# Kernel optimization log

Hardware: AMD Instinct MI355X
Metric: run time of the kernel (lower is better)

Reference implementation:

```python
import jax, jax.numpy as jnp
import numpy as np

B, T, S_ENC, D = 2, 1024, 1024, 2048
NQ, NKV, H = 16, 8, 256
EPS = 1e-6
CAP = 50.0
SCALE = 0.0625  # query_pre_attn_scalar = head_dim**-0.5
BASE = 10000
K_MASK = -2.3819763e+38


def rms_norm(x, scale, eps=EPS):
    var = jnp.mean(jnp.square(x), axis=-1, keepdims=True)
    return x * jax.lax.rsqrt(var + eps) * (1.0 + scale)


def apply_rope(x, positions, base=BASE):
    # x: [B, L, N, H], positions: [B, L] float. rope_proportion=1.0 -> full head.
    head_dim = x.shape[-1]
    timescale = base ** (2.0 / head_dim * jnp.arange(head_dim // 2, dtype=jnp.float32))
    sinusoid = positions[..., None] / timescale  # [B, L, H/2]
    sinusoid = sinusoid[..., None, :]            # [B, L, 1, H/2]
    sin, cos = jnp.sin(sinusoid), jnp.cos(sinusoid)
    x1, x2 = jnp.split(x, 2, axis=-1)
    return jnp.concatenate([x1 * cos - x2 * sin, x2 * cos + x1 * sin], axis=-1).astype(x.dtype)


def setup_inputs() -> dict:
    key = jax.random.key(0)
    ks = jax.random.split(key, 6)
    hidden_states = jax.random.normal(ks[0], (B, T, D), jnp.float32)
    encoder_hidden_states = jax.random.normal(ks[1], (B, S_ENC, D), jnp.float32)
    position_ids = jnp.broadcast_to(jnp.arange(T, dtype=jnp.int32), (B, T))
    causal = jnp.tril(jnp.ones((T, T), bool))
    merged = jnp.concatenate([causal, jnp.ones((T, S_ENC), bool)], axis=-1)
    merged_attention_mask = jnp.broadcast_to(merged[None, None], (B, 1, T, T + S_ENC))
    q_w = jax.random.normal(ks[2], (NQ, D, H), jnp.float32) * 0.02
    k_w = jax.random.normal(ks[3], (NKV, D, H), jnp.float32) * 0.02
    v_w = jax.random.normal(ks[4], (NKV, D, H), jnp.float32) * 0.02
    o_w = jax.random.normal(ks[5], (NQ, H, D), jnp.float32) * 0.02
    q_scale = jnp.zeros((H,), jnp.float32)
    k_scale = jnp.zeros((H,), jnp.float32)
    return {
        'hidden_states': hidden_states,
        'encoder_hidden_states': encoder_hidden_states,
        'position_ids': position_ids,
        'merged_attention_mask': merged_attention_mask,
        'q_w': q_w, 'k_w': k_w, 'v_w': v_w, 'o_w': o_w,
        'q_scale': q_scale, 'k_scale': k_scale,
    }


def reference(hidden_states, encoder_hidden_states, position_ids, merged_attention_mask,
              q_w, k_w, v_w, o_w, q_scale, k_scale):
    # Fused QKV projections
    q = jnp.einsum('BTD,NDH->BTNH', hidden_states, q_w)
    self_k = jnp.einsum('BTD,NDH->BTNH', hidden_states, k_w)
    self_v = jnp.einsum('BTD,NDH->BTNH', hidden_states, v_w)
    # QK RMSNorm
    q = rms_norm(q, q_scale)
    self_k = rms_norm(self_k, k_scale)
    # RoPE on decoder-side q/k only
    pos = position_ids.astype(jnp.float32)
    q = apply_rope(q, pos)
    self_k = apply_rope(self_k, pos)
    # Cross KV (no RoPE, k-norm applied)
    cross_k = rms_norm(jnp.einsum('BTD,NDH->BTNH', encoder_hidden_states, k_w), k_scale)
    cross_v = jnp.einsum('BTD,NDH->BTNH', encoder_hidden_states, v_w)
    # Merge KV: [B, T+S_enc, NKV, H]
    k = jnp.concatenate([self_k, cross_k], axis=1)
    v = jnp.concatenate([self_v, cross_v], axis=1)
    q = q * SCALE
    # GQA: group query heads over kv heads
    G = NQ // NKV
    qg = q.reshape(B, T, NKV, G, H)
    logits = jnp.einsum('BTKGH,BSKH->BKGTS', qg, k)
    # Logit soft-cap
    logits = CAP * jnp.tanh(logits / CAP)
    mask = merged_attention_mask[:, 0][:, None, None]  # [B,1,1,T,S_comb]
    logits = jnp.where(mask, logits, K_MASK)
    probs = jax.nn.softmax(logits, axis=-1)
    out = jnp.einsum('BKGTS,BSKH->BTKGH', probs, v).reshape(B, T, NQ, H)
    return jnp.einsum('BTNH,NHD->BTD', out, o_w)
```

## Files before the change

kernel.cpp:

```cpp
#include <hip/hip_runtime.h>
#include <hip/hip_bf16.h>
#include <stdint.h>

typedef __hip_bfloat16 bf16;
typedef __attribute__((ext_vector_type(8))) short bv8;
typedef __attribute__((ext_vector_type(4))) float f32x4;


__device__ __forceinline__ f32x4 mfma16(bv8 a, bv8 b, f32x4 c) {
  return __builtin_amdgcn_mfma_f32_16x16x32_bf16(a, b, c, 0, 0, 0);
}

__device__ __forceinline__ void gload16(const void* g, void* lds) {
  __builtin_amdgcn_global_load_lds((const __attribute__((address_space(1))) void*)g,
                                   (__attribute__((address_space(3))) void*)lds, 16, 0, 0);
}

__device__ __forceinline__ void storeC(float* p, float v) { *p = v; }
__device__ __forceinline__ void storeC(bf16* p, float v) { *p = __float2bfloat16(v); }

__global__ void cast2_f32_bf16(const float* __restrict__ a, const float* __restrict__ b,
                               bf16* __restrict__ da, bf16* __restrict__ db, int n4each) {
  int i = blockIdx.x * blockDim.x + threadIdx.x;
  const float* s;
  bf16* d;
  if (i < n4each) { s = a; d = da; }
  else            { s = b; d = db; i -= n4each; }
  float4 v = reinterpret_cast<const float4*>(s)[i];
  bf16 t[4] = {__float2bfloat16(v.x), __float2bfloat16(v.y),
               __float2bfloat16(v.z), __float2bfloat16(v.w)};
  reinterpret_cast<uint64_t*>(d)[i] = *reinterpret_cast<uint64_t*>(t);
}

__global__ void transpose_cast_qkv(const float* __restrict__ q_w, const float* __restrict__ k_w,
                                   const float* __restrict__ v_w, bf16* __restrict__ dst) {
  __shared__ float tile[32][33];
  const int z = blockIdx.z;
  const float* s = (z < 16) ? q_w + (size_t)z * 524288
                 : (z < 24) ? k_w + (size_t)(z - 16) * 524288
                            : v_w + (size_t)(z - 24) * 524288;
  bf16* d = dst + (size_t)z * 524288;
  const int R = 2048, C = 256;
  const int c0 = blockIdx.x * 32, r0 = blockIdx.y * 32;
  const int x = threadIdx.x, y = threadIdx.y;
#pragma unroll
  for (int i = 0; i < 32; i += 8)
    tile[y + i][x] = s[(size_t)(r0 + y + i) * C + c0 + x];
  __syncthreads();
#pragma unroll
  for (int i = 0; i < 32; i += 8)
    d[(size_t)(c0 + y + i) * R + r0 + x] = __float2bfloat16(tile[x][y + i]);
}

__global__ void transpose_cast(const float* __restrict__ src, bf16* __restrict__ dst,
                               int R, int C) {
  __shared__ float tile[32][33];
  const float* s = src;
  bf16* d = dst;
  const int c0 = blockIdx.x * 32, r0 = blockIdx.y * 32;
  const int x = threadIdx.x, y = threadIdx.y;
#pragma unroll
  for (int i = 0; i < 32; i += 8)
    tile[y + i][x] = s[(size_t)(r0 + y + i) * C + c0 + x];
  __syncthreads();
#pragma unroll
  for (int i = 0; i < 32; i += 8)
    d[(size_t)(c0 + y + i) * R + r0 + x] = __float2bfloat16(tile[x][y + i]);
}

__global__ void transpose_v2(const bf16* __restrict__ vself, const bf16* __restrict__ vcross,
                             bf16* __restrict__ dst) {
  __shared__ bf16 tile[32][33];
  const int z = blockIdx.z;
  const int zz = z & 15, b = zz >> 3, kvh = zz & 7;
  const bool cross = z >= 16;
  const bf16* srcb = cross ? vcross : vself;
  const int src_ld = cross ? 4096 : 8192;
  const int t0 = cross ? 1024 : 0;
  const bf16* s = srcb + (size_t)(b * 1024) * src_ld + kvh * 256;
  bf16* d = dst + (size_t)(zz * 256) * 2048 + t0;
  const int h0 = blockIdx.x * 32, tt0 = blockIdx.y * 32;
  const int x = threadIdx.x, y = threadIdx.y;
#pragma unroll
  for (int i = 0; i < 32; i += 8)
    tile[y + i][x] = s[(size_t)(tt0 + y + i) * src_ld + h0 + x];
  __syncthreads();
#pragma unroll
  for (int i = 0; i < 32; i += 8)
    d[(size_t)(h0 + y + i) * 2048 + tt0 + x] = tile[x][y + i];
}

template <typename CT>
__device__ __forceinline__ void gemm_body(const bf16* __restrict__ A, const bf16* __restrict__ Bt,
                                          CT* __restrict__ C, int N, int K,
                                          int m0, int n0, int kbase, int ksteps) {
  __shared__ __align__(16) bf16 As[128 * 32];
  __shared__ __align__(16) bf16 Bs[128 * 32];
  const int tid = threadIdx.x;
  const int w = tid >> 6, l = tid & 63;
  const int wr = w >> 1, wc = w & 1;
  const int l15 = l & 15, lhi = l >> 4;
  const bf16* ag = A + (size_t)(m0 + (tid >> 2)) * K + kbase + (tid & 3) * 8;
  const bf16* bg = Bt + (size_t)(n0 + (tid >> 2)) * K + kbase + (tid & 3) * 8;
  bf16* asw = As + w * 512;
  bf16* bsw = Bs + w * 512;
  f32x4 acc[4][4] = {};
  for (int k0 = 0; k0 < ksteps; k0 += 32) {
    gload16(ag + k0, asw);
    gload16(ag + (size_t)64 * K + k0, asw + 2048);
    gload16(bg + k0, bsw);
    gload16(bg + (size_t)64 * K + k0, bsw + 2048);
    asm volatile("s_waitcnt vmcnt(0)" ::: "memory");
    __syncthreads();
    bv8 af[4], bfv[4];
#pragma unroll
    for (int m = 0; m < 4; ++m)
      af[m] = *reinterpret_cast<const bv8*>(As + (wr * 64 + m * 16 + l15) * 32 + lhi * 8);
#pragma unroll
    for (int n = 0; n < 4; ++n)
      bfv[n] = *reinterpret_cast<const bv8*>(Bs + (wc * 64 + n * 16 + l15) * 32 + lhi * 8);
#pragma unroll
    for (int m = 0; m < 4; ++m)
#pragma unroll
      for (int n = 0; n < 4; ++n)
        acc[m][n] = mfma16(af[m], bfv[n], acc[m][n]);
    __syncthreads();
  }
  const int r0 = m0 + wr * 64 + lhi * 4;
  const int c0 = n0 + wc * 64 + l15;
#pragma unroll
  for (int m = 0; m < 4; ++m)
#pragma unroll
    for (int n = 0; n < 4; ++n) {
      f32x4 v = acc[m][n];
#pragma unroll
      for (int j = 0; j < 4; ++j)
        storeC(&C[(size_t)(r0 + m * 16 + j) * N + c0 + n * 16], v[j]);
    }
}

__launch_bounds__(256)
__global__ void gemm_proj(const bf16* __restrict__ hid, const bf16* __restrict__ enc,
                          const bf16* __restrict__ wqkvt, bf16* __restrict__ cself,
                          bf16* __restrict__ ccross) {
  const int bx = blockIdx.x;
  const bool cross = bx >= 64;
  const bf16* A = cross ? enc : hid;
  const bf16* Bt = cross ? wqkvt + 8388608 : wqkvt;
  bf16* C = cross ? ccross : cself;
  const int N = cross ? 4096 : 8192;
  const int n0 = (cross ? bx - 64 : bx) * 128;
  gemm_body<bf16>(A, Bt, C, N, 2048, blockIdx.y * 128, n0, 0, 2048);
}

__launch_bounds__(256)
__global__ void gemm_osplit(const bf16* __restrict__ A, const bf16* __restrict__ Bt,
                            float* __restrict__ out, float* __restrict__ p1) {
  float* C = blockIdx.z ? p1 : out;
  gemm_body<float>(A, Bt, C, 2048, 4096, blockIdx.y * 128, blockIdx.x * 128,
                   blockIdx.z * 2048, 2048);
}

__global__ void add_inplace(float* __restrict__ out, const float* __restrict__ p1, int n4) {
  int i = blockIdx.x * blockDim.x + threadIdx.x;
  if (i >= n4) return;
  float4 a = reinterpret_cast<float4*>(out)[i];
  float4 b = reinterpret_cast<const float4*>(p1)[i];
  a.x += b.x; a.y += b.y; a.z += b.z; a.w += b.w;
  reinterpret_cast<float4*>(out)[i] = a;
}

template <bool ROPE>
__launch_bounds__(256)
__global__ void norm_finalize(const bf16* __restrict__ src, int src_ld, int src_col0,
                              const float* __restrict__ scale,
                              const int* __restrict__ pos_ids,
                              bf16* __restrict__ dst, int nheads, int dst_S, int dst_t0,
                              float mul) {
  const int gid = blockIdx.x * 4 + (threadIdx.x >> 6);
  const int l = threadIdx.x & 63;
  const int token = gid / nheads;
  const int n = gid - token * nheads;
  const int b = token >> 10;
  const int t = token & 1023;
  const size_t soff = (size_t)token * src_ld + src_col0 + n * 256 + l * 4;
  bf16 xb[4];
  *reinterpret_cast<uint64_t*>(xb) = *reinterpret_cast<const uint64_t*>(src + soff);
  float x[4];
#pragma unroll
  for (int c = 0; c < 4; ++c) x[c] = __bfloat162float(xb[c]);
  float ss = x[0] * x[0] + x[1] * x[1] + x[2] * x[2] + x[3] * x[3];
#pragma unroll
  for (int d = 1; d < 64; d <<= 1) ss += __shfl_xor(ss, d);
  const float r = rsqrtf(ss * (1.0f / 256.0f) + 1e-6f);
  float v[4];
#pragma unroll
  for (int c = 0; c < 4; ++c) v[c] = x[c] * r * (1.0f + scale[l * 4 + c]);
  if (ROPE) {
    const float pos = (float)pos_ids[token];
    float o[4];
#pragma unroll
    for (int c = 0; c < 4; ++c) {
      const int j = (l & 31) * 4 + c;
      const float inv_ts = exp2f(-(float)j * 0.10381025296523007f);
      const float arg = pos * inv_ts;
      const float sj = sinf(arg), cj = cosf(arg);
      const float partner = __shfl_xor(v[c], 32);
      o[c] = (l < 32) ? (v[c] * cj - partner * sj) : (v[c] * cj + partner * sj);
    }
#pragma unroll
    for (int c = 0; c < 4; ++c) v[c] = o[c];
  }
  bf16 ob[4];
#pragma unroll
  for (int c = 0; c < 4; ++c) ob[c] = __float2bfloat16(v[c] * mul);
  const size_t doff = ((size_t)((b * nheads + n) * dst_S + dst_t0 + t)) * 256 + l * 4;
  *reinterpret_cast<uint64_t*>(dst + doff) = *reinterpret_cast<uint64_t*>(ob);
}

__launch_bounds__(512, 2)
__global__ void attn_kernel(const bf16* __restrict__ qb, const bf16* __restrict__ kb,
                            const bf16* __restrict__ vt, bf16* __restrict__ attn_out) {
  __shared__ __align__(16) bf16 Ks[2][64 * 256];
  __shared__ __align__(16) bf16 Vs[2][256 * 64];
  __shared__ __align__(16) bf16 pbuf[2][64 * 72];
  __shared__ float rsb[2][2][2][2][4][4];
  const int lin = blockIdx.x + 16 * blockIdx.y;
  const int kvc = (lin & 7) | (((lin >> 7) & 1) << 3);
  const int qt  = (lin >> 3) & 15;
  const int b = kvc >> 3, kvh = kvc & 7;
  const int tid = threadIdx.x, w = tid >> 6, l = tid & 63;
  const int g = w >> 2, qsp = (w >> 1) & 1, sh = w & 1, hq = w & 3;
  const int n = kvh * 2 + g;
  const int l15 = l & 15, lhi = l >> 4;
  const int xr = (l15 & 7) << 4;

  const bf16* kbase = kb + (size_t)(b * 8 + kvh) * 2048 * 256;
  const bf16* vbase = vt + (size_t)(b * 8 + kvh) * 256 * 2048;

  const bf16* ksrc[4];
  const bf16* vsrc[4];
#pragma unroll
  for (int i = 0; i < 4; ++i) {
    const int r0 = (w * 4 + i) * 2 + (l >> 5);
    const int cbs = ((l & 31) * 16) ^ ((r0 & 7) << 4);
    ksrc[i] = kbase + r0 * 256 + (cbs >> 1);
    const int h0 = (w * 4 + i) * 8 + (l >> 3);
    const int cbv = ((l & 7) * 16) ^ ((h0 & 7) << 4);
    vsrc[i] = vbase + (size_t)h0 * 2048 + (cbv >> 1);
  }

  bv8 qf[2][8];
#pragma unroll
  for (int qs2 = 0; qs2 < 2; ++qs2) {
    const bf16* qp = qb + ((size_t)(b * 16 + n) * 1024 + qt * 64 +
                           (qsp * 2 + qs2) * 16 + l15) * 256 + lhi * 8;
#pragma unroll
    for (int f = 0; f < 8; ++f) qf[qs2][f] = *reinterpret_cast<const bv8*>(qp + f * 32);
  }

  f32x4 oacc[4][4] = {};
  float rs[2][4] = {};

  const int nt = qt + 17;

#pragma unroll
  for (int i = 0; i < 4; ++i) gload16(ksrc[i], &Ks[0][(w * 4 + i) * 512]);
#pragma unroll
  for (int i = 0; i < 4; ++i) gload16(vsrc[i], &Vs[0][(w * 4 + i) * 512]);
  asm volatile("s_waitcnt vmcnt(0)" ::: "memory");
  __syncthreads();

  for (int it = 0; it < nt; ++it) {
    const int cur = it & 1;
    if (it + 1 < nt) {
      const int itn = it + 1;
      const int s1 = (itn <= qt) ? itn * 64 : 1024 + (itn - qt - 1) * 64;
#pragma unroll
      for (int i = 0; i < 4; ++i)
        gload16(ksrc[i] + (size_t)s1 * 256, &Ks[cur ^ 1][(w * 4 + i) * 512]);
#pragma unroll
      for (int i = 0; i < 4; ++i)
        gload16(vsrc[i] + s1, &Vs[cur ^ 1][(w * 4 + i) * 512]);
    }
    f32x4 lacc[2][2] = {};
    __builtin_amdgcn_s_setprio(1);
#pragma unroll
    for (int ss2 = 0; ss2 < 2; ++ss2) {
      const int rbase = ((sh * 2 + ss2) * 16 + l15) * 256;
#pragma unroll
      for (int f = 0; f < 8; ++f) {
        const int off = rbase + (((f * 64 + lhi * 16) ^ xr) >> 1);
        bv8 kf = *reinterpret_cast<const bv8*>(&Ks[cur][off]);
        lacc[0][ss2] = mfma16(qf[0][f], kf, lacc[0][ss2]);
        lacc[1][ss2] = mfma16(qf[1][f], kf, lacc[1][ss2]);
      }
    }
    __builtin_amdgcn_s_setprio(0);
    const bool diag = (it == qt);
#pragma unroll
    for (int qs2 = 0; qs2 < 2; ++qs2)
#pragma unroll
      for (int ss2 = 0; ss2 < 2; ++ss2)
#pragma unroll
        for (int j = 0; j < 4; ++j) {
          const float raw = lacc[qs2][ss2][j];
          const float e2 = __expf(raw * 0.04f);
          const bool ok = !diag ||
              ((sh * 2 + ss2) * 16 + l15 <= (qsp * 2 + qs2) * 16 + lhi * 4 + j);
          const float p = ok ? __expf(50.f - __fdividef(100.f, e2 + 1.f)) : 0.f;
          rs[qs2][j] += p;
          pbuf[g][((qsp * 2 + qs2) * 16 + lhi * 4 + j) * 72 + (sh * 2 + ss2) * 16 + l15] =
              __float2bfloat16(p);
        }
    __syncthreads();
    __builtin_amdgcn_s_setprio(1);
#pragma unroll
    for (int ks = 0; ks < 2; ++ks) {
      bv8 pa[4];
#pragma unroll
      for (int qs = 0; qs < 4; ++qs)
        pa[qs] = *reinterpret_cast<const bv8*>(&pbuf[g][(qs * 16 + l15) * 72 + ks * 32 + lhi * 8]);
#pragma unroll
      for (int i = 0; i < 4; ++i) {
        const int off = ((hq * 4 + i) * 16 + l15) * 64 + (((ks * 64 + lhi * 16) ^ xr) >> 1);
        bv8 vf = *reinterpret_cast<const bv8*>(&Vs[cur][off]);
#pragma unroll
        for (int qs = 0; qs < 4; ++qs) oacc[qs][i] = mfma16(pa[qs], vf, oacc[qs][i]);
      }
    }
    __builtin_amdgcn_s_setprio(0);
    asm volatile("s_waitcnt vmcnt(0)" ::: "memory");
    __syncthreads();
  }
#pragma unroll
  for (int qs2 = 0; qs2 < 2; ++qs2)
#pragma unroll
    for (int j = 0; j < 4; ++j) {
      float s = rs[qs2][j];
      s += __shfl_xor(s, 1);
      s += __shfl_xor(s, 2);
      s += __shfl_xor(s, 4);
      s += __shfl_xor(s, 8);
      if (l15 == 0) rsb[g][qsp][sh][qs2][j][lhi] = s;
    }
  __syncthreads();
  float invr[4][4];
#pragma unroll
  for (int qs = 0; qs < 4; ++qs)
#pragma unroll
    for (int j = 0; j < 4; ++j)
      invr[qs][j] = 1.0f / (rsb[g][qs >> 1][0][qs & 1][j][lhi] +
                            rsb[g][qs >> 1][1][qs & 1][j][lhi]);
  bf16* op = attn_out + ((size_t)(b * 1024 + qt * 64 + lhi * 4) * 4096) + n * 256 + l15;
#pragma unroll
  for (int qs = 0; qs < 4; ++qs)
#pragma unroll
    for (int i = 0; i < 4; ++i)
#pragma unroll
      for (int j = 0; j < 4; ++j)
        op[(size_t)(qs * 16 + j) * 4096 + (hq * 4 + i) * 16] =
            __float2bfloat16(oacc[qs][i][j] * invr[qs][j]);
}

extern "C" void kernel_launch(void* const* d_in, const int* in_sizes, int n_in,
                              void* d_out, int out_size, void* d_ws, size_t ws_size,
                              hipStream_t stream) {
  (void)in_sizes; (void)n_in; (void)out_size; (void)ws_size;
  const float* hidden = (const float*)d_in[0];
  const float* enc    = (const float*)d_in[1];
  const int*   pos    = (const int*)d_in[2];
  const float* q_w = (const float*)d_in[4];
  const float* k_w = (const float*)d_in[5];
  const float* v_w = (const float*)d_in[6];
  const float* o_w = (const float*)d_in[7];
  const float* q_s = (const float*)d_in[8];
  const float* k_s = (const float*)d_in[9];
  float* out = (float*)d_out;

  char* base = (char*)d_ws;
  bf16* hid_b  = (bf16*)(base + 0);
  bf16* enc_b  = (bf16*)(base + 8388608);
  bf16* qb     = (bf16*)(base + 0);
  bf16* wqkvt  = (bf16*)(base + 16777216);
  bf16* kbuf   = (bf16*)(base + 16777216);
  bf16* vtb    = (bf16*)(base + 33554432);
  bf16* owt    = (bf16*)(base + 50331648);
  bf16* cself  = (bf16*)(base + 67108864);
  bf16* attn_b = (bf16*)(base + 67108864);
  float* p1    = (float*)(base + 83886080);
  bf16* ccross = (bf16*)(base + 100663296);

  dim3 tb32(32, 8);
  cast2_f32_bf16<<<8192, 256, 0, stream>>>(hidden, enc, hid_b, enc_b, 1048576);
  transpose_cast_qkv<<<dim3(8, 64, 32), tb32, 0, stream>>>(q_w, k_w, v_w, wqkvt);
  transpose_cast<<<dim3(64, 128, 1), tb32, 0, stream>>>(o_w, owt, 4096, 2048);
  gemm_proj<<<dim3(96, 16), 256, 0, stream>>>(hid_b, enc_b, wqkvt, cself, ccross);
  norm_finalize<true><<<8192, 256, 0, stream>>>(cself, 8192, 0, q_s, pos, qb, 16, 1024, 0, 0.0625f);
  norm_finalize<true><<<4096, 256, 0, stream>>>(cself, 8192, 4096, k_s, pos, kbuf, 8, 2048, 0, 1.0f);
  norm_finalize<false><<<4096, 256, 0, stream>>>(ccross, 4096, 0, k_s, nullptr, kbuf, 8, 2048, 1024, 1.0f);
  transpose_v2<<<dim3(8, 32, 32), tb32, 0, stream>>>(cself + 6144, ccross + 2048, vtb);
  attn_kernel<<<dim3(16, 16), 512, 0, stream>>>(qb, kbuf, vtb, attn_b);
  gemm_osplit<<<dim3(16, 16, 2), 256, 0, stream>>>(attn_b, owt, out, p1);
  add_inplace<<<4096, 256, 0, stream>>>(out, p1, 1048576);
}
```

Before: 370.0 us.

## Replace projection GEMM with 256x256-tile pipelined kernel using swizzled LDS

Replaces the 128x128-tile QKV projection GEMM with a 256x256-tile, 512-thread kernel. It uses double-buffered, XOR-swizzled LDS staging via direct global-to-LDS loads, interleaves B-tile prefetch with the MFMA phases, raises wave priority around the MFMA bursts, and remaps blocks for cache locality. The goal is more data reuse per block and hiding global load latency behind compute. In exchange it uses more LDS and registers per block and gives a coarser grid of 384 blocks, which can leave the tail unevenly balanced across CUs.

```diff
diff --git a/kernel.cpp b/kernel.cpp
--- a/kernel.cpp
+++ b/kernel.cpp
@@ -139,18 +139,121 @@
     }
 }
 
-__launch_bounds__(256)
-__global__ void gemm_proj(const bf16* __restrict__ hid, const bf16* __restrict__ enc,
-                          const bf16* __restrict__ wqkvt, bf16* __restrict__ cself,
-                          bf16* __restrict__ ccross) {
-  const int bx = blockIdx.x;
-  const bool cross = bx >= 64;
-  const bf16* A = cross ? enc : hid;
-  const bf16* Bt = cross ? wqkvt + 8388608 : wqkvt;
-  bf16* C = cross ? ccross : cself;
-  const int N = cross ? 4096 : 8192;
-  const int n0 = (cross ? bx - 64 : bx) * 128;
-  gemm_body<bf16>(A, Bt, C, N, 2048, blockIdx.y * 128, n0, 0, 2048);
+__device__ __forceinline__ void stage_half(const bf16* __restrict__ G, int ldg, int row0,
+                                           int kcol0, bf16* lds, int tid) {
+#pragma unroll
+  for (int j = 0; j < 2; ++j) {
+    const int idx = tid + j * 512;
+    const int r = idx >> 3;
+    const int cb = ((idx & 7) * 16) ^ ((r & 7) << 4);
+    gload16(G + (size_t)(row0 + r) * ldg + kcol0 + (cb >> 1), lds + idx * 8);
+  }
+}
+
+__device__ __forceinline__ bv8 frag(const bf16* p, int row, int ks, int lhi, int xw) {
+  return *reinterpret_cast<const bv8*>(p + row * 64 + (((ks * 64 + lhi * 16) ^ xw) >> 1));
+}
+
+__launch_bounds__(512, 2)
+__global__ void gemm_proj256(const bf16* __restrict__ hid, const bf16* __restrict__ enc,
+                             const bf16* __restrict__ wqkvt, bf16* __restrict__ cself,
+                             bf16* __restrict__ ccross) {
+  __shared__ __align__(16) bf16 Al[2][2][128 * 64];
+  __shared__ __align__(16) bf16 Bl[2][2][128 * 64];
+  const int lin = blockIdx.x;
+  const int swz = (lin & 7) * 48 + (lin >> 3);
+  const bf16* A;
+  const bf16* Bt;
+  bf16* C;
+  int N, M0, N0;
+  if (swz < 256) {
+    A = hid; Bt = wqkvt; C = cself; N = 8192;
+    M0 = (swz >> 5) * 256; N0 = (swz & 31) * 256;
+  } else {
+    const int u = swz - 256;
+    A = enc; Bt = wqkvt + 8388608; C = ccross; N = 4096;
+    M0 = (u >> 4) * 256; N0 = (u & 15) * 256;
+  }
+  const int K = 2048, T = 32;
+  const int tid = threadIdx.x, w = tid >> 6, l = tid & 63;
+  const int wm = w >> 2, wn = w & 3;
+  const int l15 = l & 15, lhi = l >> 4;
+  const int xw = (l15 & 7) << 4;
+
+  f32x4 acc[8][4] = {};
+
+  stage_half(A, K, M0, 0, Al[0][0], tid);
+  stage_half(A, K, M0 + 128, 0, Al[0][1], tid);
+  stage_half(Bt, K, N0, 0, Bl[0][0], tid);
+  stage_half(Bt, K, N0 + 128, 0, Bl[0][1], tid);
+  stage_half(Bt, K, N0, 64, Bl[1][0], tid);
+  stage_half(Bt, K, N0 + 128, 64, Bl[1][1], tid);
+
+  for (int t = 0; t < T; ++t) {
+    const int d = t & 1;
+    const bf16* Ab = Al[d][wm];
+    const bf16* Bb = Bl[d][wn >> 1];
+    const int rb0 = (wn & 1) * 64;
+    const int k1 = (((t + 1) < T) ? (t + 1) : 0) * 64;
+    const int k2 = (((t + 2) < T) ? (t + 2) : 0) * 64;
+    stage_half(A, K, M0, k1, Al[d ^ 1][0], tid);
+    stage_half(A, K, M0 + 128, k1, Al[d ^ 1][1], tid);
+    asm volatile("s_waitcnt vmcnt(8)" ::: "memory");
+    asm volatile("s_barrier" ::: "memory");
+    bv8 bfr[4][2];
+#pragma unroll
+    for (int i = 0; i < 4; ++i)
+#pragma unroll
+      for (int ks = 0; ks < 2; ++ks)
+        bfr[i][ks] = frag(Bb, rb0 + i * 16 + l15, ks, lhi, xw);
+    {
+      bv8 af[2][2];
+#pragma unroll
+      for (int mm = 0; mm < 2; ++mm)
+#pragma unroll
+        for (int ks = 0; ks < 2; ++ks) af[mm][ks] = frag(Ab, mm * 16 + l15, ks, lhi, xw);
+      __builtin_amdgcn_s_setprio(1);
+#pragma unroll
+      for (int ks = 0; ks < 2; ++ks)
+#pragma unroll
+        for (int mm = 0; mm < 2; ++mm)
+#pragma unroll
+          for (int i = 0; i < 4; ++i)
+            acc[mm][i] = mfma16(af[mm][ks], bfr[i][ks], acc[mm][i]);
+      __builtin_amdgcn_s_setprio(0);
+    }
+    asm volatile("s_barrier" ::: "memory");
+#pragma unroll
+    for (int q = 1; q < 4; ++q) {
+      bv8 af[2][2];
+#pragma unroll
+      for (int mm = 0; mm < 2; ++mm)
+#pragma unroll
+        for (int ks = 0; ks < 2; ++ks)
+          af[mm][ks] = frag(Ab, (q * 2 + mm) * 16 + l15, ks, lhi, xw);
+      if (q == 1) stage_half(Bt, K, N0, k2, Bl[d][0], tid);
+      if (q == 2) stage_half(Bt, K, N0 + 128, k2, Bl[d][1], tid);
+      __builtin_amdgcn_s_setprio(1);
+#pragma unroll
+      for (int ks = 0; ks < 2; ++ks)
+#pragma unroll
+        for (int mm = 0; mm < 2; ++mm)
+#pragma unroll
+          for (int i = 0; i < 4; ++i)
+            acc[q * 2 + mm][i] = mfma16(af[mm][ks], bfr[i][ks], acc[q * 2 + mm][i]);
+      __builtin_amdgcn_s_setprio(0);
+      asm volatile("s_barrier" ::: "memory");
+    }
+  }
+  const int r0 = M0 + wm * 128 + lhi * 4;
+  const int c0 = N0 + wn * 64 + l15;
+#pragma unroll
+  for (int m = 0; m < 8; ++m)
+#pragma unroll
+    for (int i = 0; i < 4; ++i)
+#pragma unroll
+      for (int j = 0; j < 4; ++j)
+        C[(size_t)(r0 + m * 16 + j) * N + c0 + i * 16] = __float2bfloat16(acc[m][i][j]);
 }
 
 __launch_bounds__(256)
@@ -395,7 +498,7 @@
   cast2_f32_bf16<<<8192, 256, 0, stream>>>(hidden, enc, hid_b, enc_b, 1048576);
   transpose_cast_qkv<<<dim3(8, 64, 32), tb32, 0, stream>>>(q_w, k_w, v_w, wqkvt);
   transpose_cast<<<dim3(64, 128, 1), tb32, 0, stream>>>(o_w, owt, 4096, 2048);
-  gemm_proj<<<dim3(96, 16), 256, 0, stream>>>(hid_b, enc_b, wqkvt, cself, ccross);
+  gemm_proj256<<<384, 512, 0, stream>>>(hid_b, enc_b, wqkvt, cself, ccross);
   norm_finalize<true><<<8192, 256, 0, stream>>>(cself, 8192, 0, q_s, pos, qb, 16, 1024, 0, 0.0625f);
   norm_finalize<true><<<4096, 256, 0, stream>>>(cself, 8192, 4096, k_s, pos, kbuf, 8, 2048, 0, 1.0f);
   norm_finalize<false><<<4096, 256, 0, stream>>>(ccross, 4096, 0, k_s, nullptr, kbuf, 8, 2048, 1024, 1.0f);
```

Result: slower. 425.7 us (+15.0%).

## Merge weight transposes and norm launches, split output GEMM K four ways

Applied to the files above, without the earlier changes.

Fuses the two weight transpose-cast kernels into one launch and the three RMSNorm/RoPE finalize launches into one kernel that picks its branch by block index. The output projection GEMM now splits K into four 1024 slices instead of two, which doubles the block count for better CU occupancy, and a four-way add reduces the partials. Two of the partial buffers reuse workspace regions (q/k buffers) that are dead by then. The trade-off is extra partial-sum traffic in exchange for fewer launches and more parallelism.

```diff
diff --git a/kernel.cpp b/kernel.cpp
--- a/kernel.cpp
+++ b/kernel.cpp
@@ -32,32 +32,29 @@
   reinterpret_cast<uint64_t*>(d)[i] = *reinterpret_cast<uint64_t*>(t);
 }
 
-__global__ void transpose_cast_qkv(const float* __restrict__ q_w, const float* __restrict__ k_w,
-                                   const float* __restrict__ v_w, bf16* __restrict__ dst) {
+__global__ void transpose_all(const float* __restrict__ q_w, const float* __restrict__ k_w,
+                              const float* __restrict__ v_w, const float* __restrict__ o_w,
+                              bf16* __restrict__ wqkvt, bf16* __restrict__ owt) {
   __shared__ float tile[32][33];
-  const int z = blockIdx.z;
-  const float* s = (z < 16) ? q_w + (size_t)z * 524288
-                 : (z < 24) ? k_w + (size_t)(z - 16) * 524288
-                            : v_w + (size_t)(z - 24) * 524288;
-  bf16* d = dst + (size_t)z * 524288;
-  const int R = 2048, C = 256;
-  const int c0 = blockIdx.x * 32, r0 = blockIdx.y * 32;
-  const int x = threadIdx.x, y = threadIdx.y;
-#pragma unroll
-  for (int i = 0; i < 32; i += 8)
-    tile[y + i][x] = s[(size_t)(r0 + y + i) * C + c0 + x];
-  __syncthreads();
-#pragma unroll
-  for (int i = 0; i < 32; i += 8)
-    d[(size_t)(c0 + y + i) * R + r0 + x] = __float2bfloat16(tile[x][y + i]);
-}
-
-__global__ void transpose_cast(const float* __restrict__ src, bf16* __restrict__ dst,
-                               int R, int C) {
-  __shared__ float tile[32][33];
-  const float* s = src;
-  bf16* d = dst;
-  const int c0 = blockIdx.x * 32, r0 = blockIdx.y * 32;
+  const int bid = blockIdx.x;
+  const float* s;
+  bf16* d;
+  int R, C, c0, r0;
+  if (bid < 16384) {
+    const int z = bid >> 9;
+    const int rem = bid & 511;
+    s = (z < 16) ? q_w + (size_t)z * 524288
+      : (z < 24) ? k_w + (size_t)(z - 16) * 524288
+                 : v_w + (size_t)(z - 24) * 524288;
+    d = wqkvt + (size_t)z * 524288;
+    R = 2048; C = 256;
+    c0 = (rem & 7) * 32; r0 = (rem >> 3) * 32;
+  } else {
+    const int rem = bid - 16384;
+    s = o_w; d = owt;
+    R = 4096; C = 2048;
+    c0 = (rem & 63) * 32; r0 = (rem >> 6) * 32;
+  }
   const int x = threadIdx.x, y = threadIdx.y;
 #pragma unroll
   for (int i = 0; i < 32; i += 8)
@@ -155,32 +152,55 @@
 
 __launch_bounds__(256)
 __global__ void gemm_osplit(const bf16* __restrict__ A, const bf16* __restrict__ Bt,
-                            float* __restrict__ out, float* __restrict__ p1) {
-  float* C = blockIdx.z ? p1 : out;
+                            float* __restrict__ out, float* __restrict__ p1,
+                            float* __restrict__ p2, float* __restrict__ p3) {
+  const int z = blockIdx.z;
+  float* C = (z == 0) ? out : (z == 1) ? p1 : (z == 2) ? p2 : p3;
   gemm_body<float>(A, Bt, C, 2048, 4096, blockIdx.y * 128, blockIdx.x * 128,
-                   blockIdx.z * 2048, 2048);
-}
-
-__global__ void add_inplace(float* __restrict__ out, const float* __restrict__ p1, int n4) {
+                   z * 1024, 1024);
+}
+
+__global__ void add_inplace4(float* __restrict__ out, const float* __restrict__ p1,
+                             const float* __restrict__ p2, const float* __restrict__ p3,
+                             int n4) {
   int i = blockIdx.x * blockDim.x + threadIdx.x;
   if (i >= n4) return;
   float4 a = reinterpret_cast<float4*>(out)[i];
   float4 b = reinterpret_cast<const float4*>(p1)[i];
-  a.x += b.x; a.y += b.y; a.z += b.z; a.w += b.w;
+  float4 c = reinterpret_cast<const float4*>(p2)[i];
+  float4 d = reinterpret_cast<const float4*>(p3)[i];
+  a.x += b.x + c.x + d.x;
+  a.y += b.y + c.y + d.y;
+  a.z += b.z + c.z + d.z;
+  a.w += b.w + c.w + d.w;
   reinterpret_cast<float4*>(out)[i] = a;
 }
 
-template <bool ROPE>
 __launch_bounds__(256)
-__global__ void norm_finalize(const bf16* __restrict__ src, int src_ld, int src_col0,
-                              const float* __restrict__ scale,
-                              const int* __restrict__ pos_ids,
-                              bf16* __restrict__ dst, int nheads, int dst_S, int dst_t0,
-                              float mul) {
-  const int gid = blockIdx.x * 4 + (threadIdx.x >> 6);
+__global__ void norm_all(const bf16* __restrict__ cself, const bf16* __restrict__ ccross,
+                         const float* __restrict__ q_s, const float* __restrict__ k_s,
+                         const int* __restrict__ pos_ids,
+                         bf16* __restrict__ qb, bf16* __restrict__ kbuf) {
+  const int rid = blockIdx.x * 4 + (threadIdx.x >> 6);
   const int l = threadIdx.x & 63;
-  const int token = gid / nheads;
-  const int n = gid - token * nheads;
+  const bf16* src;
+  const float* scale;
+  bf16* dst;
+  int r, src_ld, src_col0, nheads, dst_S, dst_t0;
+  float mul;
+  bool rope;
+  if (rid < 32768) {
+    r = rid; src = cself; src_ld = 8192; src_col0 = 0; scale = q_s;
+    dst = qb; nheads = 16; dst_S = 1024; dst_t0 = 0; mul = 0.0625f; rope = true;
+  } else if (rid < 49152) {
+    r = rid - 32768; src = cself; src_ld = 8192; src_col0 = 4096; scale = k_s;
+    dst = kbuf; nheads = 8; dst_S = 2048; dst_t0 = 0; mul = 1.0f; rope = true;
+  } else {
+    r = rid - 49152; src = ccross; src_ld = 4096; src_col0 = 0; scale = k_s;
+    dst = kbuf; nheads = 8; dst_S = 2048; dst_t0 = 1024; mul = 1.0f; rope = false;
+  }
+  const int token = r / nheads;
+  const int n = r - token * nheads;
   const int b = token >> 10;
   const int t = token & 1023;
   const size_t soff = (size_t)token * src_ld + src_col0 + n * 256 + l * 4;
@@ -192,11 +212,11 @@
   float ss = x[0] * x[0] + x[1] * x[1] + x[2] * x[2] + x[3] * x[3];
 #pragma unroll
   for (int d = 1; d < 64; d <<= 1) ss += __shfl_xor(ss, d);
-  const float r = rsqrtf(ss * (1.0f / 256.0f) + 1e-6f);
+  const float rr = rsqrtf(ss * (1.0f / 256.0f) + 1e-6f);
   float v[4];
 #pragma unroll
-  for (int c = 0; c < 4; ++c) v[c] = x[c] * r * (1.0f + scale[l * 4 + c]);
-  if (ROPE) {
+  for (int c = 0; c < 4; ++c) v[c] = x[c] * rr * (1.0f + scale[l * 4 + c]);
+  if (rope) {
     const float pos = (float)pos_ids[token];
     float o[4];
 #pragma unroll
@@ -382,8 +402,10 @@
   bf16* hid_b  = (bf16*)(base + 0);
   bf16* enc_b  = (bf16*)(base + 8388608);
   bf16* qb     = (bf16*)(base + 0);
+  float* p2    = (float*)(base + 0);
   bf16* wqkvt  = (bf16*)(base + 16777216);
   bf16* kbuf   = (bf16*)(base + 16777216);
+  float* p3    = (float*)(base + 16777216);
   bf16* vtb    = (bf16*)(base + 33554432);
   bf16* owt    = (bf16*)(base + 50331648);
   bf16* cself  = (bf16*)(base + 67108864);
@@ -393,14 +415,11 @@
 
   dim3 tb32(32, 8);
   cast2_f32_bf16<<<8192, 256, 0, stream>>>(hidden, enc, hid_b, enc_b, 1048576);
-  transpose_cast_qkv<<<dim3(8, 64, 32), tb32, 0, stream>>>(q_w, k_w, v_w, wqkvt);
-  transpose_cast<<<dim3(64, 128, 1), tb32, 0, stream>>>(o_w, owt, 4096, 2048);
+  transpose_all<<<24576, tb32, 0, stream>>>(q_w, k_w, v_w, o_w, wqkvt, owt);
   gemm_proj<<<dim3(96, 16), 256, 0, stream>>>(hid_b, enc_b, wqkvt, cself, ccross);
-  norm_finalize<true><<<8192, 256, 0, stream>>>(cself, 8192, 0, q_s, pos, qb, 16, 1024, 0, 0.0625f);
-  norm_finalize<true><<<4096, 256, 0, stream>>>(cself, 8192, 4096, k_s, pos, kbuf, 8, 2048, 0, 1.0f);
-  norm_finalize<false><<<4096, 256, 0, stream>>>(ccross, 4096, 0, k_s, nullptr, kbuf, 8, 2048, 1024, 1.0f);
+  norm_all<<<16384, 256, 0, stream>>>(cself, ccross, q_s, k_s, pos, qb, kbuf);
   transpose_v2<<<dim3(8, 32, 32), tb32, 0, stream>>>(cself + 6144, ccross + 2048, vtb);
   attn_kernel<<<dim3(16, 16), 512, 0, stream>>>(qb, kbuf, vtb, attn_b);
-  gemm_osplit<<<dim3(16, 16, 2), 256, 0, stream>>>(attn_b, owt, out, p1);
-  add_inplace<<<4096, 256, 0, stream>>>(out, p1, 1048576);
-}
+  gemm_osplit<<<dim3(16, 16, 4), 256, 0, stream>>>(attn_b, owt, out, p1, p2, p3);
+  add_inplace4<<<4096, 256, 0, stream>>>(out, p1, p2, p3, 1048576);
+}
```

Result: no change. 373.8 us (+1.0%).
